# Kernel optimization log

Measured on AMD Instinct MI355X. Metric: run time of the kernel, lower is better.

## Reference

```python
import jax, jax.numpy as jnp
import numpy as np

D_MODEL = 2048
K_DIM = 128
V_DIM = 128
H = 16
B = 1
S = 2048
SCALE_BASE = 512.0
THETA = 10000.0
EPS = 1e-5


def setup_inputs() -> dict:
    key = jax.random.key(0)
    ks = jax.random.split(key, 11)
    lin = lambda k, i, o: jax.random.normal(k, (i, o), jnp.float32) * 0.02
    return {
        "x": jax.random.normal(ks[0], (B, S, D_MODEL), jnp.float32),
        "Wq": lin(ks[1], D_MODEL, K_DIM * H), "bq": jnp.zeros((K_DIM * H,), jnp.float32),
        "Wk": lin(ks[2], D_MODEL, K_DIM * H), "bk": jnp.zeros((K_DIM * H,), jnp.float32),
        "Wv": lin(ks[3], D_MODEL, V_DIM * H), "bv": jnp.zeros((V_DIM * H,), jnp.float32),
        "Wg": lin(ks[4], D_MODEL, V_DIM * H), "bg": jnp.zeros((V_DIM * H,), jnp.float32),
        "Wo": lin(ks[5], V_DIM * H, D_MODEL), "bo": jnp.zeros((D_MODEL,), jnp.float32),
    }


def _rotate_half(x):
    # interleaved pairs: (x0, x1, x2, x3, ...) -> (-x1, x0, -x3, x2, ...)
    xr = x.reshape(*x.shape[:-1], -1, 2)
    x1, x2 = xr[..., 0], xr[..., 1]
    return jnp.stack((-x2, x1), axis=-1).reshape(x.shape)


def _rope_xpos(q, k, seq_len, dim):
    pos = jnp.arange(seq_len, dtype=jnp.float32)
    inv_freq = 1.0 / (THETA ** (jnp.arange(0, dim, 2, dtype=jnp.float32) / dim))
    freqs = jnp.repeat(pos[:, None] * inv_freq[None, :], 2, axis=-1)  # (S, dim)
    cos, sin = jnp.cos(freqs), jnp.sin(freqs)
    sbase = (jnp.arange(0, dim, 2, dtype=jnp.float32) + 0.4 * dim) / (1.4 * dim)
    power = (pos - seq_len // 2) / SCALE_BASE
    scale = jnp.repeat(sbase[None, :] ** power[:, None], 2, axis=-1)  # (S, dim)
    q = (q * cos + _rotate_half(q) * sin) * scale
    k = (k * cos + _rotate_half(k) * sin) / scale
    return q, k


def reference(x, Wq, bq, Wk, bk, Wv, bv, Wg, bg, Wo, bo):
    Bb, Ss, Dd = x.shape
    heads = lambda t: t.reshape(Bb, Ss, H, -1).transpose(0, 2, 1, 3)  # (B,H,S,d)
    q = heads(x @ Wq + bq)
    k = heads(x @ Wk + bk)
    v = heads(x @ Wv + bv)
    q, k = _rope_xpos(q, k, Ss, K_DIM)
    # per-head decay gamma_h = 1 - 2^{-5-h}
    gamma = 1.0 - 2.0 ** (-5.0 - jnp.arange(H, dtype=jnp.float32))
    pos = jnp.arange(Ss, dtype=jnp.float32)
    pm = pos[:, None] - pos[None, :]  # (S,S)
    decay_mask = jnp.where(pm >= 0, gamma[:, None, None] ** jnp.maximum(pm, 0.0), 0.0)  # (H,S,S)
    scores = jnp.einsum('bhid,bhjd->bhij', q, k) * decay_mask
    ret = jnp.einsum('bhij,bhjd->bhid', scores, v)  # (B,H,S,V_DIM)
    # concat heads and GroupNorm (num_groups=H, affine=False) over flattened rows
    concat = ret.transpose(0, 2, 1, 3).reshape(Bb * Ss, H, V_DIM)
    mu = concat.mean(-1, keepdims=True)
    var = ((concat - mu) ** 2).mean(-1, keepdims=True)
    gn = ((concat - mu) / jnp.sqrt(var + EPS)).reshape(Bb, Ss, H * V_DIM)
    out = (jax.nn.silu(x @ Wg + bg) * gn) @ Wo + bo
    return out
```

## Files before the change

### kernel.cpp

```cpp
#include <hip/hip_runtime.h>
#include <hip/hip_bf16.h>

#define S 2048
#define DM 2048
#define H 16
#define HD 128

using bf16 = __hip_bfloat16;
typedef __attribute__((ext_vector_type(8))) short bf16x8;
typedef __attribute__((ext_vector_type(8))) unsigned short u16x8;
typedef __attribute__((ext_vector_type(4))) float f32x4;

__device__ __forceinline__ unsigned short f2bu(float f) {
  bf16 b = __float2bfloat16(f);
  union { bf16 b; unsigned short u; } cv; cv.b = b; return cv.u;
}
__device__ __forceinline__ float bu2f(unsigned short u) {
  union { bf16 b; unsigned short u; } cv; cv.u = u; return __bfloat162float(cv.b);
}

__device__ __forceinline__ void async_copy16(const void* g, void* l) {
  __builtin_amdgcn_global_load_lds(
      (const __attribute__((address_space(1))) void*)g,
      (__attribute__((address_space(3))) void*)l, 16, 0, 0);
}

__global__ __launch_bounds__(256) void cvt_kernel(const float* __restrict__ x,
                                                  unsigned short* __restrict__ o) {
  int i = (blockIdx.x * 256 + threadIdx.x) * 4;
  float4 v = *(const float4*)(x + i);
  ushort4 r;
  r.x = f2bu(v.x); r.y = f2bu(v.y); r.z = f2bu(v.z); r.w = f2bu(v.w);
  *(ushort4*)(o + i) = r;
}

__global__ __launch_bounds__(256) void wtrans_kernel(
    const float* __restrict__ s0, const float* __restrict__ s1, const float* __restrict__ s2,
    const float* __restrict__ s3, const float* __restrict__ s4,
    unsigned short* __restrict__ d0, unsigned short* __restrict__ d1, unsigned short* __restrict__ d2,
    unsigned short* __restrict__ d3, unsigned short* __restrict__ d4) {
  __shared__ float tile[64][65];
  int z = blockIdx.z;
  const float* src = z == 0 ? s0 : z == 1 ? s1 : z == 2 ? s2 : z == 3 ? s3 : s4;
  unsigned short* dst = z == 0 ? d0 : z == 1 ? d1 : z == 2 ? d2 : z == 3 ? d3 : d4;
  int tid = threadIdx.x;
  int by = blockIdx.y * 64;
  int bx = blockIdx.x * 64;
  int r0 = tid >> 4;
  int c0 = (tid & 15) * 4;
#pragma unroll
  for (int i = 0; i < 4; i++) {
    int row = r0 + i * 16;
    float4 t = *(const float4*)(src + (size_t)(by + row) * DM + bx + c0);
    tile[row][c0 + 0] = t.x; tile[row][c0 + 1] = t.y;
    tile[row][c0 + 2] = t.z; tile[row][c0 + 3] = t.w;
  }
  __syncthreads();
#pragma unroll
  for (int i = 0; i < 4; i++) {
    int nrow = r0 + i * 16;
    ushort4 o;
    o.x = f2bu(tile[c0 + 0][nrow]);
    o.y = f2bu(tile[c0 + 1][nrow]);
    o.z = f2bu(tile[c0 + 2][nrow]);
    o.w = f2bu(tile[c0 + 3][nrow]);
    *(ushort4*)(dst + (size_t)(bx + nrow) * DM + by + c0) = o;
  }
}

__device__ __forceinline__ void stage_half(const unsigned short* gbase, char* ldsbase, int tid) {
#pragma unroll
  for (int r = 0; r < 2; r++) {
    int a = r * 8192 + tid * 16;
    int row = a >> 7;
    int cb = (a & 127) ^ ((row & 7) << 4);
    async_copy16((const unsigned char*)(gbase + (size_t)row * DM) + cb, ldsbase + a);
  }
}

#define LDB(dst, kkofs)                                                                        \
  _Pragma("unroll") for (int nt = 0; nt < 4; ++nt) {                                           \
    int lr = blr0 + nt * 16;                                                                   \
    dst[nt] = *(const bf16x8*)(sBc + bhalf + lr * 128 + (((kkofs) + quad * 16) ^ ((lr & 7) << 4))); \
  }
#define LDA(dst, hofs, kkofs)                                                                  \
  _Pragma("unroll") for (int mt = 0; mt < 4; ++mt) {                                           \
    int lr = mt * 32 + wm * 16 + r16;                                                          \
    dst[mt] = *(const bf16x8*)(sAc + (hofs) + lr * 128 + (((kkofs) + quad * 16) ^ ((lr & 7) << 4))); \
  }
#define MFMA16(accbase, af, bf)                                                                \
  _Pragma("unroll") for (int mt = 0; mt < 4; ++mt)                                             \
    _Pragma("unroll") for (int nt = 0; nt < 4; ++nt)                                           \
      acc[accbase + mt][nt] = __builtin_amdgcn_mfma_f32_16x16x32_bf16(af[mt], bf[nt], acc[accbase + mt][nt], 0, 0, 0);

__global__ __launch_bounds__(512, 2) void gemm_qkvg_kernel(
    const unsigned short* __restrict__ A, const unsigned short* __restrict__ Bm,
    const float* __restrict__ bias0, const float* __restrict__ bias1,
    const float* __restrict__ bias2, const float* __restrict__ bias3,
    unsigned short* __restrict__ C0, unsigned short* __restrict__ C1,
    unsigned short* __restrict__ Vt, unsigned short* __restrict__ C3) {
  __shared__ alignas(16) char smem[131072];
  char* sA = smem;
  char* sB = smem + 65536;
  int tid = threadIdx.x;
  int wg = blockIdx.y * 32 + blockIdx.x;
  int swz = (wg & 7) * 32 + (wg >> 3);
  int bm = (swz >> 5) * 256;
  int bn = (swz & 31) * 256;
  int wid = tid >> 6, lane = tid & 63;
  int wm = wid >> 2, wn = wid & 3;
  int r16 = lane & 15, quad = lane >> 4;
  f32x4 acc[8][4] = {};
  const int bhalf = (wn >> 1) << 14;
  const int blr0 = ((wn & 1) << 6) + r16;

  stage_half(Bm + (size_t)bn * DM, sB, tid);
  stage_half(Bm + (size_t)(bn + 128) * DM, sB + 16384, tid);
  stage_half(A + (size_t)bm * DM, sA, tid);
  stage_half(A + (size_t)(bm + 128) * DM, sA + 16384, tid);
  asm volatile("s_waitcnt vmcnt(0)" ::: "memory");
  __builtin_amdgcn_s_barrier();

  for (int t = 0; t < 32; ++t) {
    const int buf = (t & 1) << 15;
    const int nbuf = buf ^ 32768;
    const bool more = t < 31;
    const int kn = (t + 1) * 64;
    char* sAc = sA + buf;
    char* sBc = sB + buf;
    bf16x8 a0[4], a1[4], b0[4], b1[4];

    LDB(b0, 0)
    LDA(a0, 0, 0)
    if (more) {
      stage_half(Bm + (size_t)bn * DM + kn, sB + nbuf, tid);
      stage_half(Bm + (size_t)(bn + 128) * DM + kn, sB + nbuf + 16384, tid);
      stage_half(A + (size_t)bm * DM + kn, sA + nbuf, tid);
      stage_half(A + (size_t)(bm + 128) * DM + kn, sA + nbuf + 16384, tid);
    }
    LDB(b1, 64)
    LDA(a1, 0, 64)

    asm volatile("s_waitcnt lgkmcnt(8)" ::: "memory");
    __builtin_amdgcn_sched_barrier(0);
    __builtin_amdgcn_s_setprio(1);
    MFMA16(0, a0, b0)
    __builtin_amdgcn_s_setprio(0);
    LDA(a0, 16384, 0)

    asm volatile("s_waitcnt lgkmcnt(4)" ::: "memory");
    __builtin_amdgcn_sched_barrier(0);
    __builtin_amdgcn_s_setprio(1);
    MFMA16(0, a1, b1)
    __builtin_amdgcn_s_setprio(0);
    LDA(a1, 16384, 64)

    asm volatile("s_waitcnt lgkmcnt(4)" ::: "memory");
    __builtin_amdgcn_sched_barrier(0);
    __builtin_amdgcn_s_setprio(1);
    MFMA16(4, a0, b0)
    __builtin_amdgcn_s_setprio(0);

    asm volatile("s_waitcnt lgkmcnt(0)" ::: "memory");
    __builtin_amdgcn_sched_barrier(0);
    __builtin_amdgcn_s_setprio(1);
    MFMA16(4, a1, b1)
    __builtin_amdgcn_s_setprio(0);

    asm volatile("s_waitcnt vmcnt(0)" ::: "memory");
    __builtin_amdgcn_s_barrier();
  }

  int ch = bn >> 11;
  const float* bp = ch == 0 ? bias0 : ch == 1 ? bias1 : ch == 2 ? bias2 : bias3;
  int lcb = bn & 2047;
  if (ch == 2) {
#pragma unroll
    for (int nt = 0; nt < 4; ++nt) {
      int lc = lcb + wn * 64 + nt * 16 + r16;
      float bv = bp[lc];
#pragma unroll
      for (int mt = 0; mt < 8; ++mt) {
        int m0 = bm + (mt >> 2) * 128 + (mt & 3) * 32 + wm * 16 + quad * 4;
        ushort4 o;
        o.x = f2bu(acc[mt][nt][0] + bv);
        o.y = f2bu(acc[mt][nt][1] + bv);
        o.z = f2bu(acc[mt][nt][2] + bv);
        o.w = f2bu(acc[mt][nt][3] + bv);
        *(ushort4*)(Vt + (size_t)lc * DM + m0) = o;
      }
    }
  } else {
    unsigned short* Cp = ch == 0 ? C0 : ch == 1 ? C1 : C3;
#pragma unroll
    for (int nt = 0; nt < 4; ++nt) {
      int lc = lcb + wn * 64 + nt * 16 + r16;
      float bv = bp[lc];
#pragma unroll
      for (int mt = 0; mt < 8; ++mt) {
        int m0 = bm + (mt >> 2) * 128 + (mt & 3) * 32 + wm * 16 + quad * 4;
#pragma unroll
        for (int rr = 0; rr < 4; ++rr)
          Cp[(size_t)(m0 + rr) * DM + lc] = f2bu(acc[mt][nt][rr] + bv);
      }
    }
  }
}

__device__ __forceinline__ void stage_o(const unsigned short* gA, const unsigned short* gB,
                                        char* dA, char* dB, int tid) {
#pragma unroll
  for (int r = 0; r < 4; r++) {
    int a = r * 4096 + tid * 16;
    int row = a >> 7;
    int cb = (a & 127) ^ ((row & 7) << 4);
    async_copy16((const unsigned char*)(gA + (size_t)row * DM) + cb, dA + a);
  }
#pragma unroll
  for (int r = 0; r < 2; r++) {
    int a = r * 4096 + tid * 16;
    int row = a >> 7;
    int cb = (a & 127) ^ ((row & 7) << 4);
    async_copy16((const unsigned char*)(gB + (size_t)row * DM) + cb, dB + a);
  }
}

__global__ __launch_bounds__(256) void gemm_out_kernel(
    const unsigned short* __restrict__ A, const unsigned short* __restrict__ Bp,
    const float* __restrict__ bias, float* __restrict__ C) {
  __shared__ alignas(16) char sA[2][16384];
  __shared__ alignas(16) char sB[2][8192];
  int tid = threadIdx.x;
  int wg = blockIdx.y * 32 + blockIdx.x;
  int swz = (wg & 7) * 64 + (wg >> 3);
  int bm = (swz >> 5) * 128;
  int bn = (swz & 31) * 64;
  int wid = tid >> 6, lane = tid & 63;
  int wm = wid >> 1, wn = wid & 1;
  int r16 = lane & 15, quad = lane >> 4;
  f32x4 acc[4][2] = {};

  stage_o(A + (size_t)bm * DM, Bp + (size_t)bn * DM, sA[0], sB[0], tid);
  asm volatile("s_waitcnt vmcnt(0)" ::: "memory");
  __builtin_amdgcn_s_barrier();

  for (int t = 0; t < 32; ++t) {
    int cur = t & 1;
    bool more = t < 31;
    int kn = (t + 1) * 64;
    if (more)
      stage_o(A + (size_t)bm * DM + kn, Bp + (size_t)bn * DM + kn, sA[cur ^ 1], sB[cur ^ 1], tid);
#pragma unroll
    for (int kk = 0; kk < 2; kk++) {
      bf16x8 af[4], bfr[2];
#pragma unroll
      for (int mt = 0; mt < 4; mt++) {
        int row = wm * 64 + mt * 16 + r16;
        af[mt] = *(const bf16x8*)(sA[cur] + row * 128 + ((kk * 64 + quad * 16) ^ ((row & 7) << 4)));
      }
#pragma unroll
      for (int nt = 0; nt < 2; nt++) {
        int row = wn * 32 + nt * 16 + r16;
        bfr[nt] = *(const bf16x8*)(sB[cur] + row * 128 + ((kk * 64 + quad * 16) ^ ((row & 7) << 4)));
      }
#pragma unroll
      for (int mt = 0; mt < 4; mt++)
#pragma unroll
        for (int nt = 0; nt < 2; nt++)
          acc[mt][nt] = __builtin_amdgcn_mfma_f32_16x16x32_bf16(af[mt], bfr[nt], acc[mt][nt], 0, 0, 0);
    }
    asm volatile("s_waitcnt vmcnt(0)" ::: "memory");
    __builtin_amdgcn_s_barrier();
  }
#pragma unroll
  for (int nt = 0; nt < 2; nt++) {
    int n = bn + wn * 32 + nt * 16 + r16;
    float bv = bias[n];
#pragma unroll
    for (int mt = 0; mt < 4; mt++) {
      int m0 = bm + wm * 64 + mt * 16 + quad * 4;
#pragma unroll
      for (int r = 0; r < 4; r++)
        C[(size_t)(m0 + r) * DM + n] = acc[mt][nt][r] + bv;
    }
  }
}

__global__ __launch_bounds__(256) void rope_kernel(unsigned short* __restrict__ q,
                                                   unsigned short* __restrict__ k) {
  int idx = blockIdx.x * 256 + threadIdx.x;
  int s = idx >> 10;
  int p = idx & 1023;
  int t = p & 63;
  int head = p >> 6;
  int col = (head << 7) + (t << 1);
  size_t off = (size_t)s * DM + col;
  float ang = (float)s * exp2f((float)(-2 * t) * (13.287712379549449f / 128.0f));
  float sn, cs;
  sincosf(ang, &sn, &cs);
  float sb = ((float)(2 * t) + 51.2f) * (1.0f / 179.2f);
  float power = ((float)s - 1024.0f) * (1.0f / 512.0f);
  float scale = exp2f(power * log2f(sb));
  float l2g = log2f(1.0f - exp2f((float)(-5 - head)));
  float qsc = scale * exp2f((float)s * l2g);
  float ksc = (1.0f / scale) * exp2f(-(float)s * l2g);
  unsigned int qu = *(unsigned int*)(q + off);
  float a = bu2f(qu & 0xffff), b = bu2f(qu >> 16);
  float qa = (a * cs - b * sn) * qsc;
  float qb2 = (b * cs + a * sn) * qsc;
  *(unsigned int*)(q + off) = (unsigned int)f2bu(qa) | ((unsigned int)f2bu(qb2) << 16);
  unsigned int ku = *(unsigned int*)(k + off);
  float c2 = bu2f(ku & 0xffff), d2 = bu2f(ku >> 16);
  float ka = (c2 * cs - d2 * sn) * ksc;
  float kb2 = (d2 * cs + c2 * sn) * ksc;
  *(unsigned int*)(k + off) = (unsigned int)f2bu(ka) | ((unsigned int)f2bu(kb2) << 16);
}

__device__ __forceinline__ void stage_kv(const unsigned short* __restrict__ k,
                                         const unsigned short* __restrict__ vt,
                                         int h, int J0, unsigned char* dK,
                                         unsigned char* dV, int tid) {
#pragma unroll
  for (int r = 0; r < 4; r++) {
    int a = r * 4096 + tid * 16;
    int rowk = a >> 8;
    int cbk = (a & 255) ^ ((rowk & 7) << 4);
    async_copy16((const unsigned char*)(k + (size_t)(J0 + rowk) * DM + h * HD) + cbk, dK + a);
    int rowv = a >> 7;
    int cbv = (a & 127) ^ ((rowv & 7) << 4);
    async_copy16((const unsigned char*)(vt + (size_t)(h * HD + rowv) * DM + J0) + cbv, dV + a);
  }
}

__global__ __launch_bounds__(256) void retention_kernel(
    const unsigned short* __restrict__ q, const unsigned short* __restrict__ k,
    const unsigned short* __restrict__ vt, const unsigned short* __restrict__ g,
    unsigned short* __restrict__ y) {
  __shared__ alignas(16) unsigned char sK[2][16384];
  __shared__ alignas(16) unsigned char sV[2][16384];
  __shared__ alignas(16) unsigned char Plds[8192];
  int bx = blockIdx.x;
  int hi = bx >> 8;
  int h = ((bx >> 5) & 7) | (hi << 3);
  int ib = hi ? (bx & 31) : (31 - (bx & 31));
  int I = ib << 6;
  int tid = threadIdx.x, wid = tid >> 6, lane = tid & 63;
  int r16 = lane & 15, quad = lane >> 4;
  bf16x8 aQ[4];
  size_t qrow = (size_t)(I + wid * 16 + r16);
#pragma unroll
  for (int kk = 0; kk < 4; kk++)
    aQ[kk] = *(const bf16x8*)(q + qrow * DM + h * HD + kk * 32 + quad * 8);
  f32x4 acc[8] = {};
  unsigned char* Pw = Plds + wid * 2048;
  stage_kv(k, vt, h, 0, sK[0], sV[0], tid);
  for (int J0 = 0; J0 <= I; J0 += 64) {
    int cur = (J0 >> 6) & 1;
    bool more = (J0 + 64) <= I;
    if (more) stage_kv(k, vt, h, J0 + 64, sK[cur ^ 1], sV[cur ^ 1], tid);
    if (more) { asm volatile("s_waitcnt vmcnt(8)" ::: "memory"); }
    else      { asm volatile("s_waitcnt vmcnt(0)" ::: "memory"); }
    __builtin_amdgcn_s_barrier();
    const unsigned char* sKc = sK[cur];
    const unsigned char* sVc = sV[cur];
    f32x4 sf[4] = {};
#pragma unroll
    for (int nt = 0; nt < 4; nt++) {
      int row = nt * 16 + r16;
#pragma unroll
      for (int kk = 0; kk < 4; kk++) {
        bf16x8 bK = *(const bf16x8*)(sKc + row * 256 + ((kk * 64 + quad * 16) ^ ((row & 7) << 4)));
        sf[nt] = __builtin_amdgcn_mfma_f32_16x16x32_bf16(aQ[kk], bK, sf[nt], 0, 0, 0);
      }
    }
    bool diag = (J0 == I);
#pragma unroll
    for (int nt = 0; nt < 4; nt++) {
      int j = nt * 16 + r16;
#pragma unroll
      for (int r = 0; r < 4; r++) {
        int ii = wid * 16 + quad * 4 + r;
        float pv = sf[nt][r];
        if (diag && (ii - j) < 0) pv = 0.0f;
        int pr = quad * 4 + r;
        int pcb = (nt * 16 + r16) * 2;
        *(unsigned short*)(Pw + pr * 128 + (pcb ^ ((pr & 7) << 4))) = f2bu(pv);
      }
    }
#pragma unroll
    for (int kk2 = 0; kk2 < 2; kk2++) {
      int cb = kk2 * 64 + quad * 16;
      bf16x8 aP = *(const bf16x8*)(Pw + r16 * 128 + (cb ^ ((r16 & 7) << 4)));
#pragma unroll
      for (int nt2 = 0; nt2 < 8; nt2++) {
        int row = nt2 * 16 + r16;
        bf16x8 bV = *(const bf16x8*)(sVc + row * 128 + ((kk2 * 64 + quad * 16) ^ ((row & 7) << 4)));
        acc[nt2] = __builtin_amdgcn_mfma_f32_16x16x32_bf16(aP, bV, acc[nt2], 0, 0, 0);
      }
    }
    __builtin_amdgcn_s_barrier();
  }
#pragma unroll
  for (int r = 0; r < 4; r++) {
    float sum = 0.0f, sq = 0.0f;
#pragma unroll
    for (int nt2 = 0; nt2 < 8; nt2++) {
      float v = acc[nt2][r];
      sum += v; sq += v * v;
    }
#pragma unroll
    for (int o = 1; o <= 8; o <<= 1) {
      sum += __shfl_xor(sum, o, 64);
      sq += __shfl_xor(sq, o, 64);
    }
    float mean = sum * 0.0078125f;
    float var = sq * 0.0078125f - mean * mean;
    float rstd = rsqrtf(var + 1e-5f);
    int i = I + wid * 16 + quad * 4 + r;
    size_t rowbase = (size_t)i * DM + h * HD;
#pragma unroll
    for (int nt2 = 0; nt2 < 8; nt2++) {
      int col = nt2 * 16 + r16;
      float gv = bu2f(g[rowbase + col]);
      float sg = gv / (1.0f + expf(-gv));
      float yv = sg * (acc[nt2][r] - mean) * rstd;
      y[rowbase + col] = f2bu(yv);
    }
  }
}

extern "C" void kernel_launch(void* const* d_in, const int* in_sizes, int n_in,
                              void* d_out, int out_size, void* d_ws, size_t ws_size,
                              hipStream_t stream) {
  (void)in_sizes; (void)n_in; (void)out_size; (void)ws_size;
  const float* x  = (const float*)d_in[0];
  const float* Wq = (const float*)d_in[1];
  const float* bq = (const float*)d_in[2];
  const float* Wk = (const float*)d_in[3];
  const float* bk = (const float*)d_in[4];
  const float* Wv = (const float*)d_in[5];
  const float* bv = (const float*)d_in[6];
  const float* Wg = (const float*)d_in[7];
  const float* bg = (const float*)d_in[8];
  const float* Wo = (const float*)d_in[9];
  const float* bo = (const float*)d_in[10];

  char* ws = (char*)d_ws;
  const size_t MB = 1ull << 20;
  unsigned short* xb   = (unsigned short*)(ws + 0 * MB);
  unsigned short* wcat = (unsigned short*)(ws + 8 * MB);
  unsigned short* wto  = (unsigned short*)(ws + 40 * MB);
  unsigned short* qb   = (unsigned short*)(ws + 48 * MB);
  unsigned short* kb   = (unsigned short*)(ws + 56 * MB);
  unsigned short* gb   = (unsigned short*)(ws + 72 * MB);
  unsigned short* vt   = (unsigned short*)(ws + 80 * MB);
  unsigned short* yb   = (unsigned short*)(ws + 104 * MB);

  cvt_kernel<<<4096, 256, 0, stream>>>(x, xb);
  wtrans_kernel<<<dim3(32, 32, 5), 256, 0, stream>>>(
      Wq, Wk, Wv, Wg, Wo,
      wcat, wcat + (size_t)2048 * DM, wcat + (size_t)4096 * DM, wcat + (size_t)6144 * DM, wto);
  gemm_qkvg_kernel<<<dim3(32, 8), 512, 0, stream>>>(
      xb, wcat, bq, bk, bv, bg, qb, kb, vt, gb);
  rope_kernel<<<8192, 256, 0, stream>>>(qb, kb);
  retention_kernel<<<512, 256, 0, stream>>>(qb, kb, vt, gb, yb);
  gemm_out_kernel<<<dim3(32, 16), 256, 0, stream>>>(yb, wto, bo, (float*)d_out);
}
```

Baseline: 174.9 us.

## Restructure QKVG GEMM main loop into 8-phase interleaved load/MFMA pipeline

The double-buffered K loop, which issued all four next-tile stage loads at once and ended each step with a full vmcnt(0) barrier, becomes a 16-iteration loop of eight phases. Each phase issues one half-tile global-to-LDS copy, reads LDS fragments, syncs with a barrier plus lgkmcnt wait, then runs 16 MFMAs. B is prefetched one half-step ahead in the prologue, and partial vmcnt waits replace full drains. The aim is to spread global traffic across the MFMA work and avoid pipeline drains, at the cost of more barriers per iteration and tricky vmcnt bookkeeping that could cause races.

```diff
diff --git a/kernel.cpp b/kernel.cpp
--- a/kernel.cpp
+++ b/kernel.cpp
@@ -78,20 +78,24 @@
   }
 }
 
-#define LDB(dst, kkofs)                                                                        \
-  _Pragma("unroll") for (int nt = 0; nt < 4; ++nt) {                                           \
-    int lr = blr0 + nt * 16;                                                                   \
-    dst[nt] = *(const bf16x8*)(sBc + bhalf + lr * 128 + (((kkofs) + quad * 16) ^ ((lr & 7) << 4))); \
-  }
-#define LDA(dst, hofs, kkofs)                                                                  \
-  _Pragma("unroll") for (int mt = 0; mt < 4; ++mt) {                                           \
-    int lr = mt * 32 + wm * 16 + r16;                                                          \
-    dst[mt] = *(const bf16x8*)(sAc + (hofs) + lr * 128 + (((kkofs) + quad * 16) ^ ((lr & 7) << 4))); \
-  }
-#define MFMA16(accbase, af, bf)                                                                \
-  _Pragma("unroll") for (int mt = 0; mt < 4; ++mt)                                             \
-    _Pragma("unroll") for (int nt = 0; nt < 4; ++nt)                                           \
+#define LDB4(dst, base, kkofs)                                                                     \
+  _Pragma("unroll") for (int nt = 0; nt < 4; ++nt) {                                               \
+    int lr = blr0 + nt * 16;                                                                       \
+    dst[nt] = *(const bf16x8*)((base) + bhalf + lr * 128 + (((kkofs) + quad * 16) ^ ((lr & 7) << 4))); \
+  }
+#define LDA4(dst, base, kkofs)                                                                     \
+  _Pragma("unroll") for (int mt = 0; mt < 4; ++mt) {                                               \
+    int lr = mt * 32 + wm * 16 + r16;                                                              \
+    dst[mt] = *(const bf16x8*)((base) + lr * 128 + (((kkofs) + quad * 16) ^ ((lr & 7) << 4)));     \
+  }
+#define MFMA16(accbase, af, bf)                                                                    \
+  _Pragma("unroll") for (int mt = 0; mt < 4; ++mt)                                                 \
+    _Pragma("unroll") for (int nt = 0; nt < 4; ++nt)                                               \
       acc[accbase + mt][nt] = __builtin_amdgcn_mfma_f32_16x16x32_bf16(af[mt], bf[nt], acc[accbase + mt][nt], 0, 0, 0);
+#define PHASE_SYNC()                                            \
+  __builtin_amdgcn_s_barrier();                                 \
+  asm volatile("s_waitcnt lgkmcnt(0)" ::: "memory");            \
+  __builtin_amdgcn_sched_barrier(0);
 
 __global__ __launch_bounds__(512, 2) void gemm_qkvg_kernel(
     const unsigned short* __restrict__ A, const unsigned short* __restrict__ Bm,
@@ -118,57 +122,91 @@
   stage_half(Bm + (size_t)(bn + 128) * DM, sB + 16384, tid);
   stage_half(A + (size_t)bm * DM, sA, tid);
   stage_half(A + (size_t)(bm + 128) * DM, sA + 16384, tid);
-  asm volatile("s_waitcnt vmcnt(0)" ::: "memory");
+  stage_half(Bm + (size_t)bn * DM + 64, sB + 32768, tid);
+  stage_half(Bm + (size_t)(bn + 128) * DM + 64, sB + 49152, tid);
+  asm volatile("s_waitcnt vmcnt(6)" ::: "memory");
   __builtin_amdgcn_s_barrier();
 
-  for (int t = 0; t < 32; ++t) {
-    const int buf = (t & 1) << 15;
-    const int nbuf = buf ^ 32768;
-    const bool more = t < 31;
-    const int kn = (t + 1) * 64;
-    char* sAc = sA + buf;
-    char* sBc = sB + buf;
+  for (int u = 0; u < 16; ++u) {
+    const bool more = u < 15;
+    const int k1 = (2 * u + 1) * 64;
+    const int k2 = (2 * u + 2) * 64;
+    const int k3 = (2 * u + 3) * 64;
     bf16x8 a0[4], a1[4], b0[4], b1[4];
 
-    LDB(b0, 0)
-    LDA(a0, 0, 0)
+    LDB4(b0, sB, 0)
+    LDA4(a0, sA, 0)
+    stage_half(A + (size_t)bm * DM + k1, sA + 32768, tid);
+    PHASE_SYNC()
+    __builtin_amdgcn_s_setprio(1);
+    MFMA16(0, a0, b0)
+    __builtin_amdgcn_s_setprio(0);
+
+    LDB4(b1, sB, 64)
+    LDA4(a1, sA, 64)
+    stage_half(A + (size_t)(bm + 128) * DM + k1, sA + 49152, tid);
+    asm volatile("s_waitcnt vmcnt(8)" ::: "memory");
+    PHASE_SYNC()
+    __builtin_amdgcn_s_setprio(1);
+    MFMA16(0, a1, b1)
+    __builtin_amdgcn_s_setprio(0);
+
+    LDA4(a0, sA + 16384, 0)
+    if (more) stage_half(Bm + (size_t)bn * DM + k2, sB, tid);
+    PHASE_SYNC()
+    __builtin_amdgcn_s_setprio(1);
+    MFMA16(4, a0, b0)
+    __builtin_amdgcn_s_setprio(0);
+
+    LDA4(a1, sA + 16384, 64)
     if (more) {
-      stage_half(Bm + (size_t)bn * DM + kn, sB + nbuf, tid);
-      stage_half(Bm + (size_t)(bn + 128) * DM + kn, sB + nbuf + 16384, tid);
-      stage_half(A + (size_t)bm * DM + kn, sA + nbuf, tid);
-      stage_half(A + (size_t)(bm + 128) * DM + kn, sA + nbuf + 16384, tid);
-    }
-    LDB(b1, 64)
-    LDA(a1, 0, 64)
-
-    asm volatile("s_waitcnt lgkmcnt(8)" ::: "memory");
-    __builtin_amdgcn_sched_barrier(0);
+      stage_half(Bm + (size_t)(bn + 128) * DM + k2, sB + 16384, tid);
+      asm volatile("s_waitcnt vmcnt(6)" ::: "memory");
+    } else {
+      asm volatile("s_waitcnt vmcnt(2)" ::: "memory");
+    }
+    PHASE_SYNC()
+    __builtin_amdgcn_s_setprio(1);
+    MFMA16(4, a1, b1)
+    __builtin_amdgcn_s_setprio(0);
+
+    LDB4(b0, sB + 32768, 0)
+    LDA4(a0, sA + 32768, 0)
+    if (more) stage_half(A + (size_t)bm * DM + k2, sA, tid);
+    PHASE_SYNC()
     __builtin_amdgcn_s_setprio(1);
     MFMA16(0, a0, b0)
     __builtin_amdgcn_s_setprio(0);
-    LDA(a0, 16384, 0)
-
-    asm volatile("s_waitcnt lgkmcnt(4)" ::: "memory");
-    __builtin_amdgcn_sched_barrier(0);
+
+    LDB4(b1, sB + 32768, 64)
+    LDA4(a1, sA + 32768, 64)
+    if (more) {
+      stage_half(A + (size_t)(bm + 128) * DM + k2, sA + 16384, tid);
+      asm volatile("s_waitcnt vmcnt(8)" ::: "memory");
+    } else {
+      asm volatile("s_waitcnt vmcnt(0)" ::: "memory");
+    }
+    PHASE_SYNC()
     __builtin_amdgcn_s_setprio(1);
     MFMA16(0, a1, b1)
     __builtin_amdgcn_s_setprio(0);
-    LDA(a1, 16384, 64)
-
-    asm volatile("s_waitcnt lgkmcnt(4)" ::: "memory");
-    __builtin_amdgcn_sched_barrier(0);
+
+    LDA4(a0, sA + 32768 + 16384, 0)
+    if (more) stage_half(Bm + (size_t)bn * DM + k3, sB + 32768, tid);
+    PHASE_SYNC()
     __builtin_amdgcn_s_setprio(1);
     MFMA16(4, a0, b0)
     __builtin_amdgcn_s_setprio(0);
 
-    asm volatile("s_waitcnt lgkmcnt(0)" ::: "memory");
-    __builtin_amdgcn_sched_barrier(0);
+    LDA4(a1, sA + 32768 + 16384, 64)
+    if (more) {
+      stage_half(Bm + (size_t)(bn + 128) * DM + k3, sB + 49152, tid);
+      asm volatile("s_waitcnt vmcnt(6)" ::: "memory");
+    }
+    PHASE_SYNC()
     __builtin_amdgcn_s_setprio(1);
     MFMA16(4, a1, b1)
     __builtin_amdgcn_s_setprio(0);
-
-    asm volatile("s_waitcnt vmcnt(0)" ::: "memory");
-    __builtin_amdgcn_s_barrier();
   }
 
   int ch = bn >> 11;
```

New measurement: 171.4 us. 1.02x faster.

## Shrink QKVG GEMM tiles to 128x64 and fold x conversion into weight transpose

Applied to the files above, without the earlier changes.

Replaces the 256x256-tile, 512-thread QKVG GEMM with its hand-scheduled MFMA/LDS interleaving by a simpler 128x64-tile, 256-thread kernel that reuses the output-GEMM staging routine, giving 2048 workgroups instead of 256. The x fp32-to-bf16 conversion kernel is merged into the weight transpose launch as an extra z slice, removing one launch. The smaller tiles lower per-block arithmetic intensity and raise global/LDS traffic, and the hand-tuned setprio and waitcnt scheduling is dropped, in exchange for more parallelism and occupancy.

```diff
diff --git a/kernel.cpp b/kernel.cpp
--- a/kernel.cpp
+++ b/kernel.cpp
@@ -25,29 +25,32 @@
       (__attribute__((address_space(3))) void*)l, 16, 0, 0);
 }
 
-__global__ __launch_bounds__(256) void cvt_kernel(const float* __restrict__ x,
-                                                  unsigned short* __restrict__ o) {
-  int i = (blockIdx.x * 256 + threadIdx.x) * 4;
-  float4 v = *(const float4*)(x + i);
-  ushort4 r;
-  r.x = f2bu(v.x); r.y = f2bu(v.y); r.z = f2bu(v.z); r.w = f2bu(v.w);
-  *(ushort4*)(o + i) = r;
-}
-
 __global__ __launch_bounds__(256) void wtrans_kernel(
     const float* __restrict__ s0, const float* __restrict__ s1, const float* __restrict__ s2,
     const float* __restrict__ s3, const float* __restrict__ s4,
     unsigned short* __restrict__ d0, unsigned short* __restrict__ d1, unsigned short* __restrict__ d2,
-    unsigned short* __restrict__ d3, unsigned short* __restrict__ d4) {
+    unsigned short* __restrict__ d3, unsigned short* __restrict__ d4,
+    const float* __restrict__ x, unsigned short* __restrict__ xb) {
   __shared__ float tile[64][65];
   int z = blockIdx.z;
-  const float* src = z == 0 ? s0 : z == 1 ? s1 : z == 2 ? s2 : z == 3 ? s3 : s4;
-  unsigned short* dst = z == 0 ? d0 : z == 1 ? d1 : z == 2 ? d2 : z == 3 ? d3 : d4;
   int tid = threadIdx.x;
   int by = blockIdx.y * 64;
   int bx = blockIdx.x * 64;
   int r0 = tid >> 4;
   int c0 = (tid & 15) * 4;
+  if (z == 5) {
+#pragma unroll
+    for (int i = 0; i < 4; i++) {
+      int row = by + r0 + i * 16;
+      float4 t = *(const float4*)(x + (size_t)row * DM + bx + c0);
+      ushort4 o;
+      o.x = f2bu(t.x); o.y = f2bu(t.y); o.z = f2bu(t.z); o.w = f2bu(t.w);
+      *(ushort4*)(xb + (size_t)row * DM + bx + c0) = o;
+    }
+    return;
+  }
+  const float* src = z == 0 ? s0 : z == 1 ? s1 : z == 2 ? s2 : z == 3 ? s3 : s4;
+  unsigned short* dst = z == 0 ? d0 : z == 1 ? d1 : z == 2 ? d2 : z == 3 ? d3 : d4;
 #pragma unroll
   for (int i = 0; i < 4; i++) {
     int row = r0 + i * 16;
@@ -68,105 +71,71 @@
   }
 }
 
-__device__ __forceinline__ void stage_half(const unsigned short* gbase, char* ldsbase, int tid) {
-#pragma unroll
-  for (int r = 0; r < 2; r++) {
-    int a = r * 8192 + tid * 16;
+__device__ __forceinline__ void stage_o(const unsigned short* gA, const unsigned short* gB,
+                                        char* dA, char* dB, int tid) {
+#pragma unroll
+  for (int r = 0; r < 4; r++) {
+    int a = r * 4096 + tid * 16;
     int row = a >> 7;
     int cb = (a & 127) ^ ((row & 7) << 4);
-    async_copy16((const unsigned char*)(gbase + (size_t)row * DM) + cb, ldsbase + a);
-  }
-}
-
-#define LDB(dst, kkofs)                                                                        \
-  _Pragma("unroll") for (int nt = 0; nt < 4; ++nt) {                                           \
-    int lr = blr0 + nt * 16;                                                                   \
-    dst[nt] = *(const bf16x8*)(sBc + bhalf + lr * 128 + (((kkofs) + quad * 16) ^ ((lr & 7) << 4))); \
-  }
-#define LDA(dst, hofs, kkofs)                                                                  \
-  _Pragma("unroll") for (int mt = 0; mt < 4; ++mt) {                                           \
-    int lr = mt * 32 + wm * 16 + r16;                                                          \
-    dst[mt] = *(const bf16x8*)(sAc + (hofs) + lr * 128 + (((kkofs) + quad * 16) ^ ((lr & 7) << 4))); \
-  }
-#define MFMA16(accbase, af, bf)                                                                \
-  _Pragma("unroll") for (int mt = 0; mt < 4; ++mt)                                             \
-    _Pragma("unroll") for (int nt = 0; nt < 4; ++nt)                                           \
-      acc[accbase + mt][nt] = __builtin_amdgcn_mfma_f32_16x16x32_bf16(af[mt], bf[nt], acc[accbase + mt][nt], 0, 0, 0);
-
-__global__ __launch_bounds__(512, 2) void gemm_qkvg_kernel(
+    async_copy16((const unsigned char*)(gA + (size_t)row * DM) + cb, dA + a);
+  }
+#pragma unroll
+  for (int r = 0; r < 2; r++) {
+    int a = r * 4096 + tid * 16;
+    int row = a >> 7;
+    int cb = (a & 127) ^ ((row & 7) << 4);
+    async_copy16((const unsigned char*)(gB + (size_t)row * DM) + cb, dB + a);
+  }
+}
+
+__global__ __launch_bounds__(256) void gemm_qkvg_kernel(
     const unsigned short* __restrict__ A, const unsigned short* __restrict__ Bm,
     const float* __restrict__ bias0, const float* __restrict__ bias1,
     const float* __restrict__ bias2, const float* __restrict__ bias3,
     unsigned short* __restrict__ C0, unsigned short* __restrict__ C1,
     unsigned short* __restrict__ Vt, unsigned short* __restrict__ C3) {
-  __shared__ alignas(16) char smem[131072];
-  char* sA = smem;
-  char* sB = smem + 65536;
+  __shared__ alignas(16) char sA[2][16384];
+  __shared__ alignas(16) char sB[2][8192];
   int tid = threadIdx.x;
-  int wg = blockIdx.y * 32 + blockIdx.x;
-  int swz = (wg & 7) * 32 + (wg >> 3);
-  int bm = (swz >> 5) * 256;
-  int bn = (swz & 31) * 256;
+  int wg = blockIdx.y * 128 + blockIdx.x;
+  int swz = (wg & 7) * 256 + (wg >> 3);
+  int bm = (swz >> 7) * 128;
+  int bn = (swz & 127) * 64;
   int wid = tid >> 6, lane = tid & 63;
-  int wm = wid >> 2, wn = wid & 3;
+  int wm = wid >> 1, wn = wid & 1;
   int r16 = lane & 15, quad = lane >> 4;
-  f32x4 acc[8][4] = {};
-  const int bhalf = (wn >> 1) << 14;
-  const int blr0 = ((wn & 1) << 6) + r16;
-
-  stage_half(Bm + (size_t)bn * DM, sB, tid);
-  stage_half(Bm + (size_t)(bn + 128) * DM, sB + 16384, tid);
-  stage_half(A + (size_t)bm * DM, sA, tid);
-  stage_half(A + (size_t)(bm + 128) * DM, sA + 16384, tid);
+  f32x4 acc[4][2] = {};
+
+  stage_o(A + (size_t)bm * DM, Bm + (size_t)bn * DM, sA[0], sB[0], tid);
   asm volatile("s_waitcnt vmcnt(0)" ::: "memory");
   __builtin_amdgcn_s_barrier();
 
   for (int t = 0; t < 32; ++t) {
-    const int buf = (t & 1) << 15;
-    const int nbuf = buf ^ 32768;
-    const bool more = t < 31;
-    const int kn = (t + 1) * 64;
-    char* sAc = sA + buf;
-    char* sBc = sB + buf;
-    bf16x8 a0[4], a1[4], b0[4], b1[4];
-
-    LDB(b0, 0)
-    LDA(a0, 0, 0)
-    if (more) {
-      stage_half(Bm + (size_t)bn * DM + kn, sB + nbuf, tid);
-      stage_half(Bm + (size_t)(bn + 128) * DM + kn, sB + nbuf + 16384, tid);
-      stage_half(A + (size_t)bm * DM + kn, sA + nbuf, tid);
-      stage_half(A + (size_t)(bm + 128) * DM + kn, sA + nbuf + 16384, tid);
-    }
-    LDB(b1, 64)
-    LDA(a1, 0, 64)
-
-    asm volatile("s_waitcnt lgkmcnt(8)" ::: "memory");
-    __builtin_amdgcn_sched_barrier(0);
-    __builtin_amdgcn_s_setprio(1);
-    MFMA16(0, a0, b0)
-    __builtin_amdgcn_s_setprio(0);
-    LDA(a0, 16384, 0)
-
-    asm volatile("s_waitcnt lgkmcnt(4)" ::: "memory");
-    __builtin_amdgcn_sched_barrier(0);
-    __builtin_amdgcn_s_setprio(1);
-    MFMA16(0, a1, b1)
-    __builtin_amdgcn_s_setprio(0);
-    LDA(a1, 16384, 64)
-
-    asm volatile("s_waitcnt lgkmcnt(4)" ::: "memory");
-    __builtin_amdgcn_sched_barrier(0);
-    __builtin_amdgcn_s_setprio(1);
-    MFMA16(4, a0, b0)
-    __builtin_amdgcn_s_setprio(0);
-
-    asm volatile("s_waitcnt lgkmcnt(0)" ::: "memory");
-    __builtin_amdgcn_sched_barrier(0);
-    __builtin_amdgcn_s_setprio(1);
-    MFMA16(4, a1, b1)
-    __builtin_amdgcn_s_setprio(0);
-
+    int cur = t & 1;
+    bool more = t < 31;
+    int kn = (t + 1) * 64;
+    if (more)
+      stage_o(A + (size_t)bm * DM + kn, Bm + (size_t)bn * DM + kn, sA[cur ^ 1], sB[cur ^ 1], tid);
+#pragma unroll
+    for (int kk = 0; kk < 2; kk++) {
+      bf16x8 af[4], bfr[2];
+#pragma unroll
+      for (int mt = 0; mt < 4; mt++) {
+        int row = wm * 64 + mt * 16 + r16;
+        af[mt] = *(const bf16x8*)(sA[cur] + row * 128 + ((kk * 64 + quad * 16) ^ ((row & 7) << 4)));
+      }
+#pragma unroll
+      for (int nt = 0; nt < 2; nt++) {
+        int row = wn * 32 + nt * 16 + r16;
+        bfr[nt] = *(const bf16x8*)(sB[cur] + row * 128 + ((kk * 64 + quad * 16) ^ ((row & 7) << 4)));
+      }
+#pragma unroll
+      for (int mt = 0; mt < 4; mt++)
+#pragma unroll
+        for (int nt = 0; nt < 2; nt++)
+          acc[mt][nt] = __builtin_amdgcn_mfma_f32_16x16x32_bf16(af[mt], bfr[nt], acc[mt][nt], 0, 0, 0);
+    }
     asm volatile("s_waitcnt vmcnt(0)" ::: "memory");
     __builtin_amdgcn_s_barrier();
   }
@@ -176,12 +145,12 @@
   int lcb = bn & 2047;
   if (ch == 2) {
 #pragma unroll
-    for (int nt = 0; nt < 4; ++nt) {
-      int lc = lcb + wn * 64 + nt * 16 + r16;
+    for (int nt = 0; nt < 2; ++nt) {
+      int lc = lcb + wn * 32 + nt * 16 + r16;
       float bv = bp[lc];
 #pragma unroll
-      for (int mt = 0; mt < 8; ++mt) {
-        int m0 = bm + (mt >> 2) * 128 + (mt & 3) * 32 + wm * 16 + quad * 4;
+      for (int mt = 0; mt < 4; ++mt) {
+        int m0 = bm + wm * 64 + mt * 16 + quad * 4;
         ushort4 o;
         o.x = f2bu(acc[mt][nt][0] + bv);
         o.y = f2bu(acc[mt][nt][1] + bv);
@@ -193,35 +162,17 @@
   } else {
     unsigned short* Cp = ch == 0 ? C0 : ch == 1 ? C1 : C3;
 #pragma unroll
-    for (int nt = 0; nt < 4; ++nt) {
-      int lc = lcb + wn * 64 + nt * 16 + r16;
+    for (int nt = 0; nt < 2; ++nt) {
+      int lc = lcb + wn * 32 + nt * 16 + r16;
       float bv = bp[lc];
 #pragma unroll
-      for (int mt = 0; mt < 8; ++mt) {
-        int m0 = bm + (mt >> 2) * 128 + (mt & 3) * 32 + wm * 16 + quad * 4;
+      for (int mt = 0; mt < 4; ++mt) {
+        int m0 = bm + wm * 64 + mt * 16 + quad * 4;
 #pragma unroll
         for (int rr = 0; rr < 4; ++rr)
           Cp[(size_t)(m0 + rr) * DM + lc] = f2bu(acc[mt][nt][rr] + bv);
       }
     }
-  }
-}
-
-__device__ __forceinline__ void stage_o(const unsigned short* gA, const unsigned short* gB,
-                                        char* dA, char* dB, int tid) {
-#pragma unroll
-  for (int r = 0; r < 4; r++) {
-    int a = r * 4096 + tid * 16;
-    int row = a >> 7;
-    int cb = (a & 127) ^ ((row & 7) << 4);
-    async_copy16((const unsigned char*)(gA + (size_t)row * DM) + cb, dA + a);
-  }
-#pragma unroll
-  for (int r = 0; r < 2; r++) {
-    int a = r * 4096 + tid * 16;
-    int row = a >> 7;
-    int cb = (a & 127) ^ ((row & 7) << 4);
-    async_copy16((const unsigned char*)(gB + (size_t)row * DM) + cb, dB + a);
   }
 }
 
@@ -456,11 +407,11 @@
   unsigned short* vt   = (unsigned short*)(ws + 80 * MB);
   unsigned short* yb   = (unsigned short*)(ws + 104 * MB);
 
-  cvt_kernel<<<4096, 256, 0, stream>>>(x, xb);
-  wtrans_kernel<<<dim3(32, 32, 5), 256, 0, stream>>>(
+  wtrans_kernel<<<dim3(32, 32, 6), 256, 0, stream>>>(
       Wq, Wk, Wv, Wg, Wo,
-      wcat, wcat + (size_t)2048 * DM, wcat + (size_t)4096 * DM, wcat + (size_t)6144 * DM, wto);
-  gemm_qkvg_kernel<<<dim3(32, 8), 512, 0, stream>>>(
+      wcat, wcat + (size_t)2048 * DM, wcat + (size_t)4096 * DM, wcat + (size_t)6144 * DM, wto,
+      x, xb);
+  gemm_qkvg_kernel<<<dim3(128, 16), 256, 0, stream>>>(
       xb, wcat, bq, bk, bv, bg, qb, kb, vt, gb);
   rope_kernel<<<8192, 256, 0, stream>>>(qb, kb);
   retention_kernel<<<512, 256, 0, stream>>>(qb, kb, vt, gb, yb);
```

New measurement: 204.7 us. 17.1% more time.
